# Performance work log

Measured on AMD Instinct MI355X. Metric: run time of the kernel, lower is better.

## Reference

```python
import math
import jax, jax.numpy as jnp
from jax import lax
import numpy as np

B, DIM, H, W = 8, 256, 64, 64
D_STATE, D_CONV, EXPAND = 16, 4, 2
D_INNER = EXPAND * DIM
DT_RANK = math.ceil(DIM / 16)
POS_LEN = 16
EPS = 1e-5
GN_GROUPS = 32


def setup_inputs() -> dict:
    key = jax.random.key(0)
    ks = iter(jax.random.split(key, 24))
    rn = lambda shape, s=0.02: jax.random.normal(next(ks), shape, jnp.float32) * s
    inp = {}
    inp["x"] = jax.random.normal(next(ks), (B, DIM, H, W), jnp.float32)
    inp["pos_emb"] = rn((1, DIM, POS_LEN), 1.0)
    inp["ln_g"] = jnp.ones((DIM,), jnp.float32)
    inp["ln_b"] = jnp.zeros((DIM,), jnp.float32)
    inp["m_in_w"] = rn((2, 2 * D_INNER, DIM))
    inp["m_conv_w"] = rn((2, D_INNER, D_CONV), 0.1)
    inp["m_conv_b"] = jnp.zeros((2, D_INNER), jnp.float32)
    inp["m_xproj_w"] = rn((2, DT_RANK + 2 * D_STATE, D_INNER))
    inp["m_dt_w"] = rn((2, D_INNER, DT_RANK), 0.1)
    inp["m_dt_b"] = rn((2, D_INNER), 0.1)
    inp["m_A_log"] = jnp.tile(jnp.log(jnp.arange(1, D_STATE + 1, dtype=jnp.float32))[None, None, :], (2, D_INNER, 1))
    inp["m_D"] = jnp.ones((2, D_INNER), jnp.float32)
    inp["m_out_w"] = rn((2, DIM, D_INNER))
    inp["proj_w"] = rn((DIM, 2 * DIM))
    inp["proj_b"] = jnp.zeros((DIM,), jnp.float32)
    inp["up_dw_w"] = rn((DIM, 1, 3, 3), 0.1)
    inp["up_bn1_g"] = jnp.ones((DIM,), jnp.float32)
    inp["up_bn1_b"] = jnp.zeros((DIM,), jnp.float32)
    inp["up_pw_w"] = rn((DIM, DIM), 0.05)
    inp["up_bn2_g"] = jnp.ones((DIM,), jnp.float32)
    inp["up_bn2_b"] = jnp.zeros((DIM,), jnp.float32)
    inp["down_pw_w"] = rn((DIM, DIM), 0.05)
    inp["down_bn_g"] = jnp.ones((DIM,), jnp.float32)
    inp["down_bn_b"] = jnp.zeros((DIM,), jnp.float32)
    inp["gn_g"] = jnp.ones((DIM,), jnp.float32)
    inp["gn_b"] = jnp.zeros((DIM,), jnp.float32)
    return inp


def reference(x, pos_emb, ln_g, ln_b, m_in_w, m_conv_w, m_conv_b, m_xproj_w, m_dt_w, m_dt_b,
              m_A_log, m_D, m_out_w, proj_w, proj_b, up_dw_w, up_bn1_g, up_bn1_b, up_pw_w,
              up_bn2_g, up_bn2_b, down_pw_w, down_bn_g, down_bn_b, gn_g, gn_b):
    Bx, C, Hh, Ww = x.shape

    def ln(t):  # LayerNorm over last dim (shared self.norm)
        m = jnp.mean(t, -1, keepdims=True)
        v = jnp.mean((t - m) ** 2, -1, keepdims=True)
        return (t - m) * lax.rsqrt(v + EPS) * ln_g + ln_b

    def bn(t, g, b):  # BatchNorm2d in eval mode with default running stats (mean 0, var 1)
        return t * (g / jnp.sqrt(1.0 + EPS))[None, :, None, None] + b[None, :, None, None]

    def gn(t):  # GroupNorm(32, C), shared params (self.bn)
        Bn, Cn, Hn, Wn = t.shape
        tg = t.reshape(Bn, GN_GROUPS, Cn // GN_GROUPS, Hn, Wn)
        m = jnp.mean(tg, (2, 3, 4), keepdims=True)
        v = jnp.mean((tg - m) ** 2, (2, 3, 4), keepdims=True)
        tg = (tg - m) * lax.rsqrt(v + EPS)
        return tg.reshape(Bn, Cn, Hn, Wn) * gn_g[None, :, None, None] + gn_b[None, :, None, None]

    def interp_pos(N):  # F.interpolate(pos_embed, size=N, mode='linear', align_corners=False)
        coords = jnp.maximum((jnp.arange(N, dtype=jnp.float32) + 0.5) * (POS_LEN / N) - 0.5, 0.0)
        i0 = jnp.floor(coords).astype(jnp.int32)
        i1 = jnp.minimum(i0 + 1, POS_LEN - 1)
        wgt = coords - i0.astype(jnp.float32)
        return pos_emb[:, :, i0] * (1.0 - wgt) + pos_emb[:, :, i1] * wgt  # (1,C,N)

    def pe_branch(vals, idx, N):  # vals (B,C,N); indices interp at same size = identity
        t = vals + interp_pos(N) + idx.astype(jnp.float32)
        return ln(jnp.swapaxes(t, 1, 2))  # (B,N,C)

    def mamba(u, d):  # standard mamba_ssm selective scan; u (B,L,C)
        xz = jnp.einsum('blc,ic->bli', u, m_in_w[d])
        xh, zg = jnp.split(xz, 2, -1)
        xc = lax.conv_general_dilated(jnp.swapaxes(xh, 1, 2), m_conv_w[d][:, None, :], (1,),
                                      [(D_CONV - 1, 0)], feature_group_count=D_INNER,
                                      dimension_numbers=('NCH', 'OIH', 'NCH'))
        xc = jnp.swapaxes(jax.nn.silu(xc + m_conv_b[d][None, :, None]), 1, 2)  # (B,L,di)
        dbl = jnp.einsum('bld,ed->ble', xc, m_xproj_w[d])
        dt = dbl[..., :DT_RANK]
        Bm = dbl[..., DT_RANK:DT_RANK + D_STATE]
        Cm = dbl[..., DT_RANK + D_STATE:]
        dt = jax.nn.softplus(jnp.einsum('blr,dr->bld', dt, m_dt_w[d]) + m_dt_b[d])  # (B,L,di)
        A = -jnp.exp(m_A_log[d])  # (di,ds)
        dA = jnp.exp(dt[..., None] * A)  # (B,L,di,ds)
        dBx = dt[..., None] * Bm[:, :, None, :] * xc[..., None]

        def step(h, inps):
            dA_t, dBx_t, C_t = inps
            h = dA_t * h + dBx_t
            return h, jnp.einsum('bds,bs->bd', h, C_t)

        h0 = jnp.zeros((u.shape[0], D_INNER, D_STATE), u.dtype)
        _, ys = lax.scan(step, h0, (jnp.swapaxes(dA, 0, 1), jnp.swapaxes(dBx, 0, 1), jnp.swapaxes(Cm, 0, 1)))
        y = jnp.swapaxes(ys, 0, 1) + xc * m_D[d]
        y = y * jax.nn.silu(zg)
        return jnp.einsum('bld,od->blo', y, m_out_w[d])

    # z branch: depthwise ConvTranspose2d(k3,s2,p1,op1) + BN + ReLU + pw conv + BN, then ReLU6
    z = lax.conv_general_dilated(x, jnp.flip(up_dw_w, (2, 3)), (1, 1), [(1, 2), (1, 2)],
                                 lhs_dilation=(2, 2), feature_group_count=C,
                                 dimension_numbers=('NCHW', 'OIHW', 'NCHW'))  # (B,C,2H,2W)
    z = jax.nn.relu(bn(z, up_bn1_g, up_bn1_b))
    z = jnp.einsum('bchw,oc->bohw', z, up_pw_w)
    z = jnp.clip(bn(z, up_bn2_g, up_bn2_b), 0.0, 6.0)

    col_max = pe_branch(jnp.max(x, 2), jnp.argmax(x, 2), Ww)
    col_min = pe_branch(jnp.min(x, 2), jnp.argmin(x, 2), Ww)
    row_max = pe_branch(jnp.max(x, 3), jnp.argmax(x, 3), Hh)
    row_min = pe_branch(jnp.min(x, 3), jnp.argmin(x, 3), Hh)
    result_max = jnp.concatenate([col_max, row_max], 1)  # (B, W+H, C)
    result_min = jnp.concatenate([col_min, row_min], 1)

    fm_max = ln(mamba(result_max, 0))
    fm_min = ln(mamba(result_min, 0))
    bm_max = ln(mamba(jnp.flip(result_max, 1), 1))
    bm_min = ln(mamba(jnp.flip(result_min, 1), 1))

    res_max = jnp.concatenate([fm_max, jnp.flip(bm_max, 1)], -1) @ proj_w.T + proj_b
    res_min = jnp.concatenate([fm_min, jnp.flip(bm_min, 1)], -1) @ proj_w.T + proj_b
    res_max = ln(res_max)[:, :, None, :]  # (B,L,1,C)
    res_min = ln(res_min)[:, None, :, :]  # (B,1,L,C)

    res = jnp.transpose(res_max + res_min, (0, 3, 1, 2))  # (B,C,L,L), L=H+W=2H
    res = jnp.clip(res + 3.0, 0.0, 6.0) / 6.0 * z  # h_sigmoid gate
    res = gn(res)
    res = jnp.einsum('bchw,oc->bohw', res[:, :, ::2, ::2], down_pw_w)  # pw conv stride 2
    res = bn(res, down_bn_g, down_bn_b)
    res = gn(res)
    res = res + x
    res = gn(res)
    return res
```

## Files before the change

kernel.cpp:

```cpp
#include <hip/hip_runtime.h>
#include <hip/hip_bf16.h>
#include <math.h>

typedef __hip_bfloat16 bf16;
typedef __attribute__((ext_vector_type(8))) short short8_t;
typedef __attribute__((ext_vector_type(4))) short short4_t;
typedef __attribute__((ext_vector_type(4))) float f32x4_t;

#define EPSV 1e-5f
#define BNSC 0.99999500003749968f

__device__ __forceinline__ float bf2f(bf16 v){ return __bfloat162float(v); }
__device__ __forceinline__ bf16 f2bf(float v){ return __float2bfloat16(v); }

__device__ __forceinline__ float blk_sum(float v, float* sm){
  int tid = threadIdx.x;
  #pragma unroll
  for(int o=32;o>0;o>>=1) v += __shfl_down(v, o, 64);
  if((tid&63)==0) sm[tid>>6] = v;
  __syncthreads();
  float s = 0.f;
  int nw = blockDim.x>>6;
  for(int i=0;i<nw;i++) s += sm[i];
  __syncthreads();
  return s;
}

__device__ __forceinline__ float softplusf(float x){
  return (x > 20.f) ? x : __logf(1.f + __expf(x));
}
__device__ __forceinline__ float siluf(float x){
  return x / (1.f + __expf(-x));
}

__global__ void prep_weights(const float* __restrict__ in_w, const float* __restrict__ out_w,
                             const float* __restrict__ pw_w, const float* __restrict__ dpw_w,
                             const float* __restrict__ proj_w,
                             bf16* __restrict__ Winb, bf16* __restrict__ Woutb,
                             bf16* __restrict__ Wub, bf16* __restrict__ Wdb,
                             float* __restrict__ PT, float* __restrict__ gacc){
  int idx = blockIdx.x*256 + threadIdx.x;
  if(idx < 1536) gacc[idx] = 0.f;
  if(idx < 524288){ Winb[idx] = f2bf(in_w[idx]); return; }
  if(idx < 786432){ int i=idx-524288; Woutb[i] = f2bf(out_w[i]); return; }
  if(idx < 851968){ int i=idx-786432; Wub[i] = f2bf(pw_w[i]); return; }
  if(idx < 917504){ int i=idx-851968; Wdb[i] = f2bf(dpw_w[i]); return; }
  int k = idx - 917504;
  int i = k >> 9, j = k & 511;
  PT[j*256 + i] = proj_w[k];
}

__global__ __launch_bounds__(256)
void r1_reduce_pe(const float* __restrict__ x, const float* __restrict__ pe,
                  float* __restrict__ pmax, float* __restrict__ pmin){
  __shared__ float tile[64*65];
  int bc = blockIdx.x;
  int b = bc >> 8, c = bc & 255;
  const float* xp = x + ((size_t)bc << 12);
  for(int i=threadIdx.x; i<4096; i+=256)
    tile[(i>>6)*65 + (i&63)] = xp[i];
  __syncthreads();
  int wv = threadIdx.x >> 6, t = threadIdx.x & 63;
  if(wv >= 2) return;
  float coords = fmaxf((t + 0.5f)*0.25f - 0.5f, 0.f);
  int i0 = (int)floorf(coords);
  int i1 = min(i0+1, 15);
  float wg = coords - (float)i0;
  float pos = pe[c*16+i0]*(1.f-wg) + pe[c*16+i1]*wg;
  if(wv == 0){
    float cmx=-3.4e38f, cmn=3.4e38f; int cax=0, can=0;
    for(int h=0;h<64;h++){
      float v = tile[h*65 + t];
      if(v > cmx){ cmx=v; cax=h; }
      if(v < cmn){ cmn=v; can=h; }
    }
    size_t base_col = ((size_t)b*128 + t)*256 + c;
    pmax[base_col] = cmx + pos + (float)cax;
    pmin[base_col] = cmn + pos + (float)can;
  } else {
    float rmx=-3.4e38f, rmn=3.4e38f; int rax=0, ran=0;
    for(int w=0;w<64;w++){
      float v = tile[t*65 + w];
      if(v > rmx){ rmx=v; rax=w; }
      if(v < rmn){ rmn=v; ran=w; }
    }
    size_t base_row = ((size_t)b*128 + 64 + t)*256 + c;
    pmax[base_row] = rmx + pos + (float)rax;
    pmin[base_row] = rmn + pos + (float)ran;
  }
}

__global__ void ln_rows2(float* __restrict__ bufA, float* __restrict__ bufB,
                         const float* __restrict__ g, const float* __restrict__ bb,
                         bf16* __restrict__ boutA, bf16* __restrict__ boutB){
  __shared__ float sm[8];
  int row = blockIdx.x, t = threadIdx.x;
  float* buf; bf16* bout;
  if(row < 1024){ buf = bufA; bout = boutA; }
  else { buf = bufB; bout = boutB; row -= 1024; }
  float v = buf[(size_t)row*256 + t];
  float m = blk_sum(v, sm) * (1.f/256.f);
  float dv = v - m;
  float var = blk_sum(dv*dv, sm) * (1.f/256.f);
  float r = dv * rsqrtf(var + EPSV) * g[t] + bb[t];
  buf[(size_t)row*256 + t] = r;
  if(bout) bout[(size_t)row*256 + t] = f2bf(r);
}

__global__ __launch_bounds__(256,2)
void m1_mfma(const bf16* __restrict__ ubmax, const bf16* __restrict__ ubmin,
             const bf16* __restrict__ Win, float* __restrict__ xz){
  __shared__ bf16 att[64*264];
  int bx = blockIdx.x;
  int it = bx & 3, lt = (bx>>2)&1, b = (bx>>3)&7, r = bx>>6;
  int d = r & 1;
  const bf16* u = (r < 2) ? ubmax : ubmin;
  int flip = r & 1;
  int t = threadIdx.x;
  {
    int pr = t>>5, cc = (t&31)*8;
    #pragma unroll
    for(int i=0;i<8;i++){
      int p = pr + i*8;
      int l = lt*64 + p;
      int le = flip ? (127 - l) : l;
      short8_t v = *(const short8_t*)((const short*)u + ((size_t)(b*128 + le))*256 + cc);
      *(short8_t*)&att[p*264 + cc] = v;
    }
  }
  __syncthreads();
  int wv = t>>6, lane = t&63, quad = lane>>4, l16 = lane&15;
  int m0 = wv*64;
  f32x4_t acc[4][4];
  #pragma unroll
  for(int ms=0;ms<4;ms++)
    #pragma unroll
    for(int ns=0;ns<4;ns++) acc[ms][ns] = (f32x4_t){0.f,0.f,0.f,0.f};
  const short* wbase = (const short*)Win + ((size_t)d*1024 + it*256)*256;
  for(int k0=0;k0<256;k0+=32){
    short8_t afr[4], bfr[4];
    #pragma unroll
    for(int ms=0;ms<4;ms++)
      afr[ms] = *(const short8_t*)(wbase + (size_t)(m0 + ms*16 + l16)*256 + k0 + quad*8);
    #pragma unroll
    for(int ns=0;ns<4;ns++)
      bfr[ns] = *(const short8_t*)&att[(ns*16 + l16)*264 + k0 + quad*8];
    #pragma unroll
    for(int ms=0;ms<4;ms++)
      #pragma unroll
      for(int ns=0;ns<4;ns++)
        acc[ms][ns] = __builtin_amdgcn_mfma_f32_16x16x32_bf16(afr[ms], bfr[ns], acc[ms][ns], 0,0,0);
  }
  int rb = r*8 + b;
  #pragma unroll
  for(int ns=0;ns<4;ns++){
    int l = lt*64 + ns*16 + l16;
    float* dst = xz + ((size_t)rb*128 + l)*1024 + it*256;
    #pragma unroll
    for(int ms=0;ms<4;ms++){
      int i = m0 + ms*16 + quad*4;
      *(f32x4_t*)(dst + i) = acc[ms][ns];
    }
  }
}

#define LSEG 8
__global__ __launch_bounds__(256)
void m234(const float* __restrict__ xz, const float* __restrict__ cw,
          const float* __restrict__ cb, const float* __restrict__ xproj,
          const float* __restrict__ dtw, const float* __restrict__ dtbias,
          float* __restrict__ xc, float* __restrict__ dbl, float* __restrict__ dt){
  __shared__ float xzs[(LSEG+3)*512];
  __shared__ float xcs[LSEG*512];
  __shared__ float pbuf[LSEG*96];
  __shared__ float dblrow[LSEG*48];
  int bx = blockIdx.x;
  int rb = bx >> 4, seg = bx & 15;
  int l0 = seg * LSEG;
  int d = (rb >> 3) & 1;
  int t = threadIdx.x;
  #pragma unroll
  for(int j=0; j<(LSEG+3)*512/256; j++){
    int i = t + j*256;
    int r = i >> 9, dd = i & 511;
    int ls = l0 - 3 + r;
    xzs[i] = (ls >= 0) ? xz[((size_t)rb*128 + ls)*1024 + dd] : 0.f;
  }
  __syncthreads();
  #pragma unroll
  for(int j=0; j<(LSEG*512)/256; j++){
    int i = t + j*256;
    int lr = i >> 9, dd = i & 511;
    f32x4_t wv = *(const f32x4_t*)(cw + (size_t)(d*512 + dd)*4);
    float s = cb[d*512 + dd];
    s += xzs[(lr+0)*512 + dd]*wv[0];
    s += xzs[(lr+1)*512 + dd]*wv[1];
    s += xzs[(lr+2)*512 + dd]*wv[2];
    s += xzs[(lr+3)*512 + dd]*wv[3];
    s = siluf(s);
    xcs[i] = s;
    xc[((size_t)(rb*128 + l0 + lr))*512 + dd] = s;
  }
  __syncthreads();
  #pragma unroll
  for(int j=0; j<3; j++){
    int id = t + j*256;
    int row = id / 96;
    int rem = id - row*96;
    int e = rem >> 1, part = rem & 1;
    const float* wp = xproj + ((size_t)(d*48 + e)*512) + part*256;
    const float* xr = xcs + row*512 + part*256;
    float s = 0.f;
    #pragma unroll 4
    for(int k4=0; k4<64; k4++){
      f32x4_t wv = *(const f32x4_t*)(wp + k4*4);
      f32x4_t xv = *(const f32x4_t*)(xr + k4*4);
      s += wv[0]*xv[0] + wv[1]*xv[1] + wv[2]*xv[2] + wv[3]*xv[3];
    }
    pbuf[id] = s;
  }
  __syncthreads();
  for(int i=t; i<LSEG*48; i+=256){
    float s = pbuf[2*i] + pbuf[2*i+1];
    dblrow[i] = s;
    int row = i / 48, e = i - row*48;
    dbl[((size_t)(rb*128 + l0 + row))*48 + e] = s;
  }
  __syncthreads();
  #pragma unroll
  for(int j=0; j<(LSEG*512)/256; j++){
    int i = t + j*256;
    int row = i >> 9, dd = i & 511;
    const float* wp = dtw + (size_t)(d*512 + dd)*16;
    const float* dr = dblrow + row*48;
    float s = dtbias[d*512 + dd];
    #pragma unroll
    for(int r4=0; r4<4; r4++){
      f32x4_t wv = *(const f32x4_t*)(wp + r4*4);
      s += dr[r4*4+0]*wv[0] + dr[r4*4+1]*wv[1] + dr[r4*4+2]*wv[2] + dr[r4*4+3]*wv[3];
    }
    dt[((size_t)(rb*128 + l0 + row))*512 + dd] = softplusf(s);
  }
}

__global__ void m5_passA(const float* __restrict__ dt, const float* __restrict__ xc,
                         const float* __restrict__ dbl, const float* __restrict__ Alog,
                         float* __restrict__ P, float* __restrict__ Hl){
  int bx = blockIdx.x;
  int seg = bx & 7, half = (bx>>3)&1, rb = bx>>4;
  int dd = half*256 + threadIdx.x;
  int d = (rb>>3)&1;
  float A[16], h[16], pr[16];
  #pragma unroll
  for(int s=0;s<16;s++){
    A[s] = -__expf(Alog[(size_t)(d*512 + dd)*16 + s]);
    h[s] = 0.f; pr[s] = 1.f;
  }
  int l0 = seg*16;
  for(int l=l0;l<l0+16;l++){
    size_t row = (size_t)rb*128 + l;
    float dtv = dt[row*512 + dd];
    float xcv = xc[row*512 + dd];
    float bx_ = dtv*xcv;
    const float* dr = dbl + row*48;
    #pragma unroll
    for(int s=0;s<16;s++){
      float dA = __expf(dtv*A[s]);
      pr[s] *= dA;
      h[s] = dA*h[s] + bx_*dr[16+s];
    }
  }
  size_t o = ((size_t)(rb*8 + seg)*512 + dd)*16;
  #pragma unroll
  for(int s=0;s<16;s+=4){
    *(f32x4_t*)(P  + o + s) = (f32x4_t){pr[s],pr[s+1],pr[s+2],pr[s+3]};
    *(f32x4_t*)(Hl + o + s) = (f32x4_t){h[s],h[s+1],h[s+2],h[s+3]};
  }
}

__global__ void m5_passB(const float* __restrict__ dt, const float* __restrict__ xc,
                         const float* __restrict__ dbl, const float* __restrict__ xz,
                         const float* __restrict__ Alog, const float* __restrict__ Dp,
                         const float* __restrict__ P, const float* __restrict__ Hl,
                         bf16* __restrict__ ybb){
  int bx = blockIdx.x;
  int seg = bx & 7, half = (bx>>3)&1, rb = bx>>4;
  int dd = half*256 + threadIdx.x;
  int d = (rb>>3)&1;
  float A[16], h[16];
  #pragma unroll
  for(int s=0;s<16;s++){
    A[s] = -__expf(Alog[(size_t)(d*512 + dd)*16 + s]);
    h[s] = 0.f;
  }
  for(int j=0;j<seg;j++){
    size_t o = ((size_t)(rb*8 + j)*512 + dd)*16;
    #pragma unroll
    for(int s=0;s<16;s+=4){
      f32x4_t pv = *(const f32x4_t*)(P + o + s);
      f32x4_t hv = *(const f32x4_t*)(Hl + o + s);
      h[s]   = pv[0]*h[s]   + hv[0];
      h[s+1] = pv[1]*h[s+1] + hv[1];
      h[s+2] = pv[2]*h[s+2] + hv[2];
      h[s+3] = pv[3]*h[s+3] + hv[3];
    }
  }
  float Dv = Dp[d*512 + dd];
  int l0 = seg*16;
  for(int l=l0;l<l0+16;l++){
    size_t row = (size_t)rb*128 + l;
    float dtv = dt[row*512 + dd];
    float xcv = xc[row*512 + dd];
    float zgv = xz[row*1024 + 512 + dd];
    const float* dr = dbl + row*48;
    float bx_ = dtv*xcv;
    float y = 0.f;
    #pragma unroll
    for(int s=0;s<16;s++){
      h[s] = __expf(dtv*A[s])*h[s] + bx_*dr[16+s];
      y += h[s]*dr[32+s];
    }
    ybb[row*512 + dd] = f2bf((y + xcv*Dv) * siluf(zgv));
  }
}

__global__ __launch_bounds__(256,2)
void m6_mfma(const bf16* __restrict__ ybb, const bf16* __restrict__ Wout,
             const float* __restrict__ lng, const float* __restrict__ lnb,
             float* __restrict__ mo){
  __shared__ char smem[64*264*4];
  bf16* ybt = (bf16*)smem;
  float* fbuf = (float*)smem;
  int bx = blockIdx.x;
  int lt = bx & 1, b = (bx>>1)&7, r = bx>>4;
  int d = r & 1, rb = r*8 + b;
  size_t rowbase = (size_t)rb*128 + lt*64;
  int t = threadIdx.x;
  for(int i=t;i<4096;i+=256){
    int row = i>>6, c8 = (i&63)*8;
    short8_t v = *(const short8_t*)((const short*)ybb + (rowbase + row)*512 + c8);
    *(short8_t*)&ybt[row*520 + c8] = v;
  }
  __syncthreads();
  int wv = t>>6, lane = t&63, quad = lane>>4, l16 = lane&15;
  int m0 = wv*64;
  f32x4_t acc[4][4];
  #pragma unroll
  for(int ms=0;ms<4;ms++)
    #pragma unroll
    for(int ns=0;ns<4;ns++) acc[ms][ns] = (f32x4_t){0.f,0.f,0.f,0.f};
  const short* wbase = (const short*)Wout + (size_t)d*256*512;
  for(int k0=0;k0<512;k0+=32){
    short8_t afr[4], bfr[4];
    #pragma unroll
    for(int ms=0;ms<4;ms++)
      afr[ms] = *(const short8_t*)(wbase + (size_t)(m0 + ms*16 + l16)*512 + k0 + quad*8);
    #pragma unroll
    for(int ns=0;ns<4;ns++)
      bfr[ns] = *(const short8_t*)&ybt[(ns*16 + l16)*520 + k0 + quad*8];
    #pragma unroll
    for(int ms=0;ms<4;ms++)
      #pragma unroll
      for(int ns=0;ns<4;ns++)
        acc[ms][ns] = __builtin_amdgcn_mfma_f32_16x16x32_bf16(afr[ms], bfr[ns], acc[ms][ns], 0,0,0);
  }
  __syncthreads();
  #pragma unroll
  for(int ns=0;ns<4;ns++){
    int row = ns*16 + l16;
    #pragma unroll
    for(int ms=0;ms<4;ms++){
      int o = m0 + ms*16 + quad*4;
      *(f32x4_t*)(fbuf + row*264 + o) = acc[ms][ns];
    }
  }
  __syncthreads();
  {
    int row = t >> 2, part = t & 3;
    const float* fr = fbuf + row*264;
    float s = 0.f;
    #pragma unroll 8
    for(int j=0;j<64;j++){
      int col = part*64 + ((j + part*16) & 63);
      s += fr[col];
    }
    s += __shfl_xor(s, 1, 64);
    s += __shfl_xor(s, 2, 64);
    float m = s * (1.f/256.f);
    float q = 0.f;
    #pragma unroll 8
    for(int j=0;j<64;j++){
      int col = part*64 + ((j + part*16) & 63);
      float dv = fr[col] - m;
      q += dv*dv;
    }
    q += __shfl_xor(q, 1, 64);
    q += __shfl_xor(q, 2, 64);
    float rs = rsqrtf(q*(1.f/256.f) + EPSV);
    float* dst = mo + (rowbase + row)*256;
    for(int j=0;j<64;j++){
      int col = part*64 + j;
      dst[col] = (fr[col] - m)*rs*lng[col] + lnb[col];
    }
  }
}

__global__ void m7_proj(const float* __restrict__ mo, const float* __restrict__ PT,
                        const float* __restrict__ pb, const float* __restrict__ lng,
                        const float* __restrict__ lnb, float* __restrict__ resm,
                        float* __restrict__ resn){
  __shared__ float ct[16*512];
  __shared__ float fbuf[16*264];
  int bx = blockIdx.x;
  int tt = bx >> 6, rem = bx & 63, b = rem >> 3, lt = rem & 7;
  int fr_ = tt*2, br = tt*2 + 1;
  for(int i=threadIdx.x;i<16*512;i+=256){
    int lr = i >> 9, k = i & 511;
    int l = lt*16 + lr;
    ct[i] = (k < 256)
      ? mo[(((size_t)(fr_*8+b)*128) + l)*256 + k]
      : mo[(((size_t)(br*8+b)*128) + (127-l))*256 + (k-256)];
  }
  __syncthreads();
  float acc[16];
  #pragma unroll
  for(int q=0;q<16;q++) acc[q] = 0.f;
  int t = threadIdx.x;
  for(int k=0;k<512;k++){
    float pv = PT[(size_t)k*256 + t];
    #pragma unroll
    for(int q=0;q<16;q++) acc[q] += pv * ct[(q<<9) + k];
  }
  float bias = pb[t];
  #pragma unroll
  for(int q=0;q<16;q++) fbuf[q*264 + t] = acc[q] + bias;
  __syncthreads();
  float* dstbuf = tt ? resn : resm;
  if(t < 64){
    int row = t >> 2, part = t & 3;
    const float* fr = fbuf + row*264;
    float s = 0.f;
    for(int j=0;j<64;j++){
      int col = part*64 + ((j + part*16) & 63);
      s += fr[col];
    }
    s += __shfl_xor(s, 1, 64);
    s += __shfl_xor(s, 2, 64);
    float m = s * (1.f/256.f);
    float q = 0.f;
    for(int j=0;j<64;j++){
      int col = part*64 + ((j + part*16) & 63);
      float dv = fr[col] - m;
      q += dv*dv;
    }
    q += __shfl_xor(q, 1, 64);
    q += __shfl_xor(q, 2, 64);
    float rs = rsqrtf(q*(1.f/256.f) + EPSV);
    float* dst = dstbuf + ((size_t)b*128 + lt*16 + row)*256;
    for(int j=0;j<64;j++){
      int col = part*64 + j;
      dst[col] = (fr[col] - m)*rs*lng[col] + lnb[col];
    }
  }
}

__global__ __launch_bounds__(256)
void k1_deconv_T(const float* __restrict__ x, const float* __restrict__ wdw,
                 const float* __restrict__ g1, const float* __restrict__ b1,
                 bf16* __restrict__ zT){
  __shared__ float in[2*64*33];
  __shared__ bf16 ot[64*80];
  int bx = blockIdx.x;
  int cb = bx & 3, half = (bx>>2)&1, h = (bx>>3)&127, b = bx>>10;
  int c0 = cb*64, w0 = half*64, iw0 = w0>>1;
  int h_odd = h & 1;
  int ihA = h_odd ? (h-1)>>1 : h>>1;
  int ihB = (h+1)>>1;
  bool hasB = h_odd && (ihB < 64);
  for(int i = threadIdx.x; i < 4224; i += 256){
    int row = i / 2112;
    int rem = i - row*2112;
    int c = rem / 33;
    int iw = rem - c*33;
    int ihl = row ? ihB : ihA;
    bool valid = (iw0 + iw < 64) && (row == 0 || hasB);
    in[i] = valid ? x[(((size_t)b*256 + c0 + c)<<12) + (ihl<<6) + iw0 + iw] : 0.f;
  }
  __syncthreads();
  int c = threadIdx.x & 63, g = threadIdx.x >> 6;
  const float* wp = wdw + (c0+c)*9;
  int khA3 = h_odd ? 6 : 3;
  float wA0 = wp[khA3], wA1 = wp[khA3+1], wA2 = wp[khA3+2];
  float wB0 = wp[0],    wB1 = wp[1],      wB2 = wp[2];
  float scale = g1[c0+c]*BNSC, bias = b1[c0+c];
  const float* inA = in + c*33;
  const float* inB = in + 2112 + c*33;
  #pragma unroll
  for(int i=0;i<16;i++){
    int wi = g*16 + i;
    float s;
    if(!(i&1)){
      int iw = wi>>1;
      s = inA[iw]*wA1 + inB[iw]*wB1;
    } else {
      int iwa = (wi-1)>>1, iwb = (wi+1)>>1;
      s = inA[iwa]*wA2 + inA[iwb]*wA0 + inB[iwa]*wB2 + inB[iwb]*wB0;
    }
    ot[wi*80 + c] = f2bf(fmaxf(s*scale + bias, 0.f));
  }
  __syncthreads();
  int rr = threadIdx.x >> 3;
  int co = (threadIdx.x & 7) * 8;
  size_t obase = (((size_t)b*16384) + (size_t)h*128 + w0)*256 + c0;
  #pragma unroll
  for(int pass=0; pass<2; pass++){
    int wi = rr + pass*32;
    short8_t v = *(const short8_t*)&ot[wi*80 + co];
    *(short8_t*)((short*)zT + obase + (size_t)wi*256 + co) = v;
  }
}

__global__ __launch_bounds__(256,2)
void k2_mfma(const bf16* __restrict__ zT, const bf16* __restrict__ Wub,
             const float* __restrict__ g2, const float* __restrict__ b2,
             const float* __restrict__ resm, const float* __restrict__ resn,
             bf16* __restrict__ resS, float* __restrict__ gsum1, float* __restrict__ gssq1){
  __shared__ bf16 zt[128*264];
  __shared__ float rm_s[256];
  __shared__ float gn_s[32], gn_q[32];
  int b = blockIdx.y;
  int p0 = blockIdx.x*128;
  int h = p0 >> 7;
  int t = threadIdx.x;
  if(t < 32){ gn_s[t] = 0.f; gn_q[t] = 0.f; }
  if(t >= 64 && t < 128){
    int tt = t - 64;
    *(f32x4_t*)&rm_s[tt*4] = *(const f32x4_t*)(resm + ((size_t)b*128 + h)*256 + tt*4);
  }
  {
    const short* src = (const short*)zT + (((size_t)b*16384 + p0)*256);
    int pr = t>>5;
    int cc = (t&31)*8;
    #pragma unroll
    for(int i=0;i<16;i++){
      int p = pr + i*8;
      short8_t v = *(const short8_t*)(src + (size_t)p*256 + cc);
      *(short8_t*)&zt[p*264 + cc] = v;
    }
  }
  __syncthreads();
  int wv = t>>6, lane = t&63, quad = lane>>4, l16 = lane&15;
  int m0 = wv*64;
  f32x4_t acc[4][8];
  #pragma unroll
  for(int ms=0;ms<4;ms++)
    #pragma unroll
    for(int ns=0;ns<8;ns++) acc[ms][ns] = (f32x4_t){0.f,0.f,0.f,0.f};
  const short* wp = (const short*)Wub + (size_t)(m0 + l16)*256 + quad*8;
  short8_t afr[4];
  #pragma unroll
  for(int ms=0;ms<4;ms++) afr[ms] = *(const short8_t*)(wp + (size_t)ms*16*256);
  for(int k0=0;k0<256;k0+=32){
    short8_t anext[4];
    if(k0 + 32 < 256){
      #pragma unroll
      for(int ms=0;ms<4;ms++)
        anext[ms] = *(const short8_t*)(wp + (size_t)ms*16*256 + k0 + 32);
    }
    short8_t bfr[8];
    #pragma unroll
    for(int ns=0;ns<8;ns++)
      bfr[ns] = *(const short8_t*)&zt[(ns*16 + l16)*264 + k0 + quad*8];
    #pragma unroll
    for(int ms=0;ms<4;ms++)
      #pragma unroll
      for(int ns=0;ns<8;ns++)
        acc[ms][ns] = __builtin_amdgcn_mfma_f32_16x16x32_bf16(afr[ms], bfr[ns], acc[ms][ns], 0,0,0);
    #pragma unroll
    for(int ms=0;ms<4;ms++) afr[ms] = anext[ms];
  }
  __syncthreads();
  bool h_even = ((h & 1) == 0);
  float sg[4], qg[4];
  #pragma unroll
  for(int ms=0;ms<4;ms++){ sg[ms]=0.f; qg[ms]=0.f; }
  #pragma unroll
  for(int ns=0;ns<8;ns++){
    int pl = ns*16 + l16;
    const float* rn = resn + ((size_t)b*128 + pl)*256;
    bool store = h_even && ((pl & 1) == 0);
    #pragma unroll
    for(int ms=0;ms<4;ms++){
      int o = m0 + ms*16 + quad*4;
      f32x4_t a = acc[ms][ns];
      f32x4_t gv = *(const f32x4_t*)(g2+o);
      f32x4_t bv = *(const f32x4_t*)(b2+o);
      f32x4_t rmv = *(const f32x4_t*)&rm_s[o];
      f32x4_t rnv = *(const f32x4_t*)(rn+o);
      alignas(8) bf16 ov[4];
      #pragma unroll
      for(int r=0;r<4;r++){
        float zv = a[r]*(gv[r]*BNSC) + bv[r];
        zv = fminf(fmaxf(zv, 0.f), 6.f);
        float gate = fminf(fmaxf(rmv[r]+rnv[r]+3.f, 0.f), 6.f)*(1.f/6.f);
        float vo = zv*gate;
        ov[r] = f2bf(vo);
        sg[ms] += vo;
        qg[ms] += vo*vo;
      }
      if(store) *(short4_t*)&zt[pl*264 + o] = *(const short4_t*)ov;
    }
  }
  #pragma unroll
  for(int ms=0;ms<4;ms++){
    float S = sg[ms], Q = qg[ms];
    S += __shfl_xor(S, 1, 64);  Q += __shfl_xor(Q, 1, 64);
    S += __shfl_xor(S, 2, 64);  Q += __shfl_xor(Q, 2, 64);
    S += __shfl_xor(S, 4, 64);  Q += __shfl_xor(Q, 4, 64);
    S += __shfl_xor(S, 8, 64);  Q += __shfl_xor(Q, 8, 64);
    if(l16 == 0){
      int o = m0 + ms*16 + quad*4;
      atomicAdd(&gn_s[o>>3], S);
      atomicAdd(&gn_q[o>>3], Q);
    }
  }
  __syncthreads();
  if(t < 32){
    atomicAdd(&gsum1[b*32 + t], gn_s[t]);
    atomicAdd(&gssq1[b*32 + t], gn_q[t]);
  }
  if(h_even){
    short* dst = (short*)resS + ((size_t)b*4096 + (h>>1)*64)*256;
    #pragma unroll
    for(int it=0; it<8; it++){
      int slot = t + it*256;
      int row = slot >> 5;
      int co = (slot & 31)*8;
      short8_t v = *(const short8_t*)&zt[(row*2)*264 + co];
      *(short8_t*)(dst + (size_t)row*256 + co) = v;
    }
  }
}

__global__ __launch_bounds__(256,2)
void k4_mfma(const bf16* __restrict__ resS, const bf16* __restrict__ Wdb,
             const float* __restrict__ gsum1, const float* __restrict__ gssq1,
             const float* __restrict__ gng, const float* __restrict__ gnb,
             const float* __restrict__ dbg, const float* __restrict__ dbb,
             float* __restrict__ t1, float* __restrict__ gsum2, float* __restrict__ gssq2){
  __shared__ bf16 at[128*264];
  __shared__ float sc[256], sb[256];
  __shared__ float stm[32], str[32];
  int b = blockIdx.y;
  int q0 = blockIdx.x*128;
  int t = threadIdx.x;
  if(t < 32){
    float m = gsum1[b*32+t] * (1.f/131072.f);
    float var = gssq1[b*32+t] * (1.f/131072.f) - m*m;
    stm[t] = m;
    str[t] = rsqrtf(var + EPSV);
  }
  __syncthreads();
  {
    int cch = t, g = cch>>3;
    float m = stm[g], rs = str[g];
    float s = rs*gng[cch];
    sc[cch] = s; sb[cch] = gnb[cch] - m*s;
  }
  __syncthreads();
  {
    int pr = t>>5;
    int cc = (t&31)*8;
    const short* src = (const short*)resS + ((size_t)b*4096 + q0)*256;
    #pragma unroll
    for(int i=0;i<16;i++){
      int q = pr + i*8;
      short8_t v = *(const short8_t*)(src + (size_t)q*256 + cc);
      const bf16* vv = (const bf16*)&v;
      alignas(16) bf16 ov[8];
      #pragma unroll
      for(int j=0;j<8;j++) ov[j] = f2bf(bf2f(vv[j])*sc[cc+j] + sb[cc+j]);
      *(short8_t*)&at[q*264 + cc] = *(const short8_t*)ov;
    }
  }
  __syncthreads();
  int wv = t>>6, lane = t&63, quad = lane>>4, l16 = lane&15;
  int n0 = wv*64;
  f32x4_t acc[8][4];
  #pragma unroll
  for(int ms=0;ms<8;ms++)
    #pragma unroll
    for(int ns=0;ns<4;ns++) acc[ms][ns] = (f32x4_t){0.f,0.f,0.f,0.f};
  const short* wp = (const short*)Wdb + (size_t)(n0 + l16)*256 + quad*8;
  short8_t bfr[4];
  #pragma unroll
  for(int ns=0;ns<4;ns++) bfr[ns] = *(const short8_t*)(wp + (size_t)ns*16*256);
  for(int k0=0;k0<256;k0+=32){
    short8_t bnext[4];
    if(k0 + 32 < 256){
      #pragma unroll
      for(int ns=0;ns<4;ns++)
        bnext[ns] = *(const short8_t*)(wp + (size_t)ns*16*256 + k0 + 32);
    }
    short8_t afr[8];
    #pragma unroll
    for(int ms=0;ms<8;ms++)
      afr[ms] = *(const short8_t*)&at[(ms*16 + l16)*264 + k0 + quad*8];
    #pragma unroll
    for(int ms=0;ms<8;ms++)
      #pragma unroll
      for(int ns=0;ns<4;ns++)
        acc[ms][ns] = __builtin_amdgcn_mfma_f32_16x16x32_bf16(afr[ms], bfr[ns], acc[ms][ns], 0,0,0);
    #pragma unroll
    for(int ns=0;ns<4;ns++) bfr[ns] = bnext[ns];
  }
  #pragma unroll
  for(int ns=0;ns<4;ns++){
    int o = n0 + ns*16 + l16;
    float s2 = dbg[o]*BNSC, bb2 = dbb[o];
    float* dst = t1 + (((size_t)b*256 + o) << 12);
    float s_=0.f, q_=0.f;
    #pragma unroll
    for(int ms=0;ms<8;ms++){
      int ps = q0 + ms*16 + quad*4;
      f32x4_t a = acc[ms][ns];
      f32x4_t ov;
      #pragma unroll
      for(int r=0;r<4;r++){
        ov[r] = a[r]*s2 + bb2;
        s_ += ov[r];
        q_ += ov[r]*ov[r];
      }
      *(f32x4_t*)(dst + ps) = ov;
    }
    #pragma unroll
    for(int msk=1; msk<=4; msk<<=1){
      s_ += __shfl_xor(s_, msk, 64);
      q_ += __shfl_xor(q_, msk, 64);
    }
    s_ += __shfl_xor(s_, 16, 64);
    q_ += __shfl_xor(q_, 16, 64);
    s_ += __shfl_xor(s_, 32, 64);
    q_ += __shfl_xor(q_, 32, 64);
    if(((l16 & 7) == 0) && (quad == 0)){
      atomicAdd(&gsum2[b*32 + (o>>3)], s_);
      atomicAdd(&gssq2[b*32 + (o>>3)], q_);
    }
  }
}

__global__ void k6_gn_add(float* __restrict__ t1, const float* __restrict__ x,
                          const float* __restrict__ gsum2, const float* __restrict__ gssq2,
                          const float* __restrict__ gng, const float* __restrict__ gnb,
                          float* __restrict__ gsum3, float* __restrict__ gssq3){
  __shared__ float sm[8];
  int i4 = blockIdx.x*256 + threadIdx.x;
  int idx = i4 << 2;
  int c = (idx >> 12) & 255, b = idx >> 20, g = c >> 3;
  float m2 = gsum2[b*32+g] * (1.f/32768.f);
  float var = gssq2[b*32+g] * (1.f/32768.f) - m2*m2;
  float rs = rsqrtf(var + EPSV);
  float scl = rs*gng[c], off = gnb[c] - m2*scl;
  f32x4_t tv = *(const f32x4_t*)(t1 + idx);
  f32x4_t xv = *(const f32x4_t*)(x + idx);
  f32x4_t ov;
  float S = 0.f, Q = 0.f;
  #pragma unroll
  for(int r=0;r<4;r++){
    float v = tv[r]*scl + off + xv[r];
    ov[r] = v;
    S += v; Q += v*v;
  }
  *(f32x4_t*)(t1 + idx) = ov;
  S = blk_sum(S, sm);
  Q = blk_sum(Q, sm);
  if(threadIdx.x == 0){
    atomicAdd(&gsum3[b*32 + g], S);
    atomicAdd(&gssq3[b*32 + g], Q);
  }
}

__global__ void k8_gn_out(const float* __restrict__ t1, const float* __restrict__ gsum3,
                          const float* __restrict__ gssq3, const float* __restrict__ gng,
                          const float* __restrict__ gnb, float* __restrict__ out){
  int i4 = blockIdx.x*256 + threadIdx.x;
  int idx = i4 << 2;
  int c = (idx >> 12) & 255, b = idx >> 20, g = c >> 3;
  float m = gsum3[b*32+g] * (1.f/32768.f);
  float var = gssq3[b*32+g] * (1.f/32768.f) - m*m;
  float rs = rsqrtf(var + EPSV);
  float scl = rs*gng[c], off = gnb[c] - m*scl;
  f32x4_t tv = *(const f32x4_t*)(t1 + idx);
  f32x4_t ov;
  #pragma unroll
  for(int r=0;r<4;r++) ov[r] = tv[r]*scl + off;
  *(f32x4_t*)(out + idx) = ov;
}

extern "C" void kernel_launch(void* const* d_in, const int* in_sizes, int n_in,
                              void* d_out, int out_size, void* d_ws, size_t ws_size,
                              hipStream_t stream){
  const float* x      = (const float*)d_in[0];
  const float* pos    = (const float*)d_in[1];
  const float* ln_g   = (const float*)d_in[2];
  const float* ln_b   = (const float*)d_in[3];
  const float* in_w   = (const float*)d_in[4];
  const float* conv_w = (const float*)d_in[5];
  const float* conv_b = (const float*)d_in[6];
  const float* xproj  = (const float*)d_in[7];
  const float* dt_w   = (const float*)d_in[8];
  const float* dt_b   = (const float*)d_in[9];
  const float* A_log  = (const float*)d_in[10];
  const float* Dp     = (const float*)d_in[11];
  const float* out_w  = (const float*)d_in[12];
  const float* proj_w = (const float*)d_in[13];
  const float* proj_b = (const float*)d_in[14];
  const float* dw_w   = (const float*)d_in[15];
  const float* bn1g   = (const float*)d_in[16];
  const float* bn1b   = (const float*)d_in[17];
  const float* pw_w   = (const float*)d_in[18];
  const float* bn2g   = (const float*)d_in[19];
  const float* bn2b   = (const float*)d_in[20];
  const float* dpw_w  = (const float*)d_in[21];
  const float* dbng   = (const float*)d_in[22];
  const float* dbnb   = (const float*)d_in[23];
  const float* gng    = (const float*)d_in[24];
  const float* gnb    = (const float*)d_in[25];
  float* out = (float*)d_out;

  float* ws = (float*)d_ws;
  bf16*  resS = (bf16*)ws;
  bf16*  zT   = (bf16*)(ws + 16777216);
  float* scanP = ws + 16777216;
  float* scanH = ws + 16777216 + 2097152;
  float* zone = ws + 33554432;
  float* xz   = zone;
  float* xc   = xz  + 4194304;
  float* dbl  = xc  + 2097152;
  float* dtb  = dbl + 196608;
  bf16*  ybb  = (bf16*)(dtb + 2097152);
  float* t1   = zone;
  float* mo   = zone + 9633792;
  float* resm = mo   + 1048576;
  float* resn = resm + 262144;
  float* pmax = resn + 262144;
  float* pmin = pmax + 262144;
  float* PT   = pmin + 262144;
  bf16*  ubmax= (bf16*)(PT + 131072);
  bf16*  ubmin= (bf16*)(PT + 131072 + 131072);
  bf16*  Winb = (bf16*)(PT + 131072 + 262144);
  bf16*  Woutb= (bf16*)(PT + 131072 + 524288);
  bf16*  Wub  = (bf16*)(PT + 131072 + 655360);
  bf16*  Wdb  = (bf16*)(PT + 131072 + 688128);
  float* gacc = PT + 131072 + 720896;
  float* gsum1 = gacc,        *gssq1 = gacc + 256;
  float* gsum2 = gacc + 512,  *gssq2 = gacc + 768;
  float* gsum3 = gacc + 1024, *gssq3 = gacc + 1280;

  prep_weights<<<4096,256,0,stream>>>(in_w, out_w, pw_w, dpw_w, proj_w,
                                      Winb, Woutb, Wub, Wdb, PT, gacc);

  r1_reduce_pe<<<2048,256,0,stream>>>(x, pos, pmax, pmin);
  ln_rows2<<<2048,256,0,stream>>>(pmax, pmin, ln_g, ln_b, ubmax, ubmin);

  m1_mfma<<<256,256,0,stream>>>(ubmax, ubmin, Winb, xz);
  m234<<<512,256,0,stream>>>(xz, conv_w, conv_b, xproj, dt_w, dt_b, xc, dbl, dtb);
  m5_passA<<<512,256,0,stream>>>(dtb, xc, dbl, A_log, scanP, scanH);
  m5_passB<<<512,256,0,stream>>>(dtb, xc, dbl, xz, A_log, Dp, scanP, scanH, ybb);
  m6_mfma<<<64,256,0,stream>>>(ybb, Woutb, ln_g, ln_b, mo);
  m7_proj<<<128,256,0,stream>>>(mo, PT, proj_b, ln_g, ln_b, resm, resn);

  k1_deconv_T<<<8192,256,0,stream>>>(x, dw_w, bn1g, bn1b, zT);
  k2_mfma<<<dim3(128,8),256,0,stream>>>(zT, Wub, bn2g, bn2b, resm, resn, resS,
                                        gsum1, gssq1);

  k4_mfma<<<dim3(32,8),256,0,stream>>>(resS, Wdb, gsum1, gssq1,
                                       gng, gnb, dbng, dbnb, t1, gsum2, gssq2);

  k6_gn_add<<<8192,256,0,stream>>>(t1, x, gsum2, gssq2, gng, gnb, gsum3, gssq3);
  k8_gn_out<<<8192,256,0,stream>>>(t1, gsum3, gssq3, gng, gnb, out);
}
```

Baseline: 502.4 us.

## Derive final GroupNorm stats algebraically and split conv/xproj kernel into finer segments

The separate residual-add plus GroupNorm pass (k6) is removed. Per-channel sums of x are computed in the first reduction kernel, and per-channel sums, squares and cross products with x are gathered in k4. A small compose kernel then derives the second and third GroupNorm statistics in closed form, so the final kernel writes out = A*t1 + B*x + C in one pass. Separately, m234 now uses 4-row segments with 1024 blocks and reads the conv taps straight from global memory, and xproj uses 4 partial sums per row instead of 2. The algebraic variance form may lose some precision, and there are more atomics per channel.

```diff
diff --git a/kernel.cpp b/kernel.cpp
--- a/kernel.cpp
+++ b/kernel.cpp
@@ -40,7 +40,7 @@
                              bf16* __restrict__ Wub, bf16* __restrict__ Wdb,
                              float* __restrict__ PT, float* __restrict__ gacc){
   int idx = blockIdx.x*256 + threadIdx.x;
-  if(idx < 1536) gacc[idx] = 0.f;
+  if(idx < 6656) gacc[idx] = 0.f;
   if(idx < 524288){ Winb[idx] = f2bf(in_w[idx]); return; }
   if(idx < 786432){ int i=idx-524288; Woutb[i] = f2bf(out_w[i]); return; }
   if(idx < 851968){ int i=idx-786432; Wub[i] = f2bf(pw_w[i]); return; }
@@ -52,15 +52,28 @@
 
 __global__ __launch_bounds__(256)
 void r1_reduce_pe(const float* __restrict__ x, const float* __restrict__ pe,
-                  float* __restrict__ pmax, float* __restrict__ pmin){
+                  float* __restrict__ pmax, float* __restrict__ pmin,
+                  float* __restrict__ xs, float* __restrict__ xq){
   __shared__ float tile[64*65];
+  __shared__ float rs_[4], rq_[4];
   int bc = blockIdx.x;
   int b = bc >> 8, c = bc & 255;
   const float* xp = x + ((size_t)bc << 12);
-  for(int i=threadIdx.x; i<4096; i+=256)
-    tile[(i>>6)*65 + (i&63)] = xp[i];
-  __syncthreads();
+  float s = 0.f, q = 0.f;
+  for(int i=threadIdx.x; i<4096; i+=256){
+    float v = xp[i];
+    tile[(i>>6)*65 + (i&63)] = v;
+    s += v; q += v*v;
+  }
+  #pragma unroll
+  for(int o=32;o>0;o>>=1){ s += __shfl_down(s, o, 64); q += __shfl_down(q, o, 64); }
   int wv = threadIdx.x >> 6, t = threadIdx.x & 63;
+  if(t == 0){ rs_[wv] = s; rq_[wv] = q; }
+  __syncthreads();
+  if(threadIdx.x == 0){
+    xs[bc] = rs_[0]+rs_[1]+rs_[2]+rs_[3];
+    xq[bc] = rq_[0]+rq_[1]+rq_[2]+rq_[3];
+  }
   if(wv >= 2) return;
   float coords = fmaxf((t + 0.5f)*0.25f - 0.5f, 0.f);
   int i0 = (int)floorf(coords);
@@ -164,55 +177,49 @@
   }
 }
 
-#define LSEG 8
+#define LSEG4 4
 __global__ __launch_bounds__(256)
 void m234(const float* __restrict__ xz, const float* __restrict__ cw,
           const float* __restrict__ cb, const float* __restrict__ xproj,
           const float* __restrict__ dtw, const float* __restrict__ dtbias,
           float* __restrict__ xc, float* __restrict__ dbl, float* __restrict__ dt){
-  __shared__ float xzs[(LSEG+3)*512];
-  __shared__ float xcs[LSEG*512];
-  __shared__ float pbuf[LSEG*96];
-  __shared__ float dblrow[LSEG*48];
+  __shared__ float xcs[LSEG4*512];
+  __shared__ float pbuf[LSEG4*48*4];
+  __shared__ float dblrow[LSEG4*48];
   int bx = blockIdx.x;
-  int rb = bx >> 4, seg = bx & 15;
-  int l0 = seg * LSEG;
+  int rb = bx >> 5, seg = bx & 31;
+  int l0 = seg * LSEG4;
   int d = (rb >> 3) & 1;
   int t = threadIdx.x;
   #pragma unroll
-  for(int j=0; j<(LSEG+3)*512/256; j++){
-    int i = t + j*256;
-    int r = i >> 9, dd = i & 511;
-    int ls = l0 - 3 + r;
-    xzs[i] = (ls >= 0) ? xz[((size_t)rb*128 + ls)*1024 + dd] : 0.f;
-  }
-  __syncthreads();
-  #pragma unroll
-  for(int j=0; j<(LSEG*512)/256; j++){
+  for(int j=0; j<(LSEG4*512)/256; j++){
     int i = t + j*256;
     int lr = i >> 9, dd = i & 511;
+    int gl = l0 + lr;
+    const float* src = xz + ((size_t)rb*128 + gl)*1024 + dd;
     f32x4_t wv = *(const f32x4_t*)(cw + (size_t)(d*512 + dd)*4);
     float s = cb[d*512 + dd];
-    s += xzs[(lr+0)*512 + dd]*wv[0];
-    s += xzs[(lr+1)*512 + dd]*wv[1];
-    s += xzs[(lr+2)*512 + dd]*wv[2];
-    s += xzs[(lr+3)*512 + dd]*wv[3];
+    float v0 = (gl >= 3) ? src[-3*1024] : 0.f;
+    float v1 = (gl >= 2) ? src[-2*1024] : 0.f;
+    float v2 = (gl >= 1) ? src[-1*1024] : 0.f;
+    float v3 = src[0];
+    s += v0*wv[0] + v1*wv[1] + v2*wv[2] + v3*wv[3];
     s = siluf(s);
     xcs[i] = s;
-    xc[((size_t)(rb*128 + l0 + lr))*512 + dd] = s;
+    xc[((size_t)(rb*128 + gl))*512 + dd] = s;
   }
   __syncthreads();
   #pragma unroll
   for(int j=0; j<3; j++){
     int id = t + j*256;
-    int row = id / 96;
-    int rem = id - row*96;
-    int e = rem >> 1, part = rem & 1;
-    const float* wp = xproj + ((size_t)(d*48 + e)*512) + part*256;
-    const float* xr = xcs + row*512 + part*256;
+    int row = id / 192;
+    int rem = id - row*192;
+    int e = rem >> 2, part = rem & 3;
+    const float* wp = xproj + ((size_t)(d*48 + e)*512) + part*128;
+    const float* xr = xcs + row*512 + part*128;
     float s = 0.f;
     #pragma unroll 4
-    for(int k4=0; k4<64; k4++){
+    for(int k4=0; k4<32; k4++){
       f32x4_t wv = *(const f32x4_t*)(wp + k4*4);
       f32x4_t xv = *(const f32x4_t*)(xr + k4*4);
       s += wv[0]*xv[0] + wv[1]*xv[1] + wv[2]*xv[2] + wv[3]*xv[3];
@@ -220,15 +227,16 @@
     pbuf[id] = s;
   }
   __syncthreads();
-  for(int i=t; i<LSEG*48; i+=256){
-    float s = pbuf[2*i] + pbuf[2*i+1];
+  for(int i=t; i<LSEG4*48; i+=256){
+    int row = i / 48, e = i - row*48;
+    int base = row*192 + e*4;
+    float s = pbuf[base] + pbuf[base+1] + pbuf[base+2] + pbuf[base+3];
     dblrow[i] = s;
-    int row = i / 48, e = i - row*48;
     dbl[((size_t)(rb*128 + l0 + row))*48 + e] = s;
   }
   __syncthreads();
   #pragma unroll
-  for(int j=0; j<(LSEG*512)/256; j++){
+  for(int j=0; j<(LSEG4*512)/256; j++){
     int i = t + j*256;
     int row = i >> 9, dd = i & 511;
     const float* wp = dtw + (size_t)(d*512 + dd)*16;
@@ -647,7 +655,8 @@
              const float* __restrict__ gsum1, const float* __restrict__ gssq1,
              const float* __restrict__ gng, const float* __restrict__ gnb,
              const float* __restrict__ dbg, const float* __restrict__ dbb,
-             float* __restrict__ t1, float* __restrict__ gsum2, float* __restrict__ gssq2){
+             const float* __restrict__ x, float* __restrict__ t1,
+             float* __restrict__ t1s, float* __restrict__ t1q, float* __restrict__ t1x){
   __shared__ bf16 at[128*264];
   __shared__ float sc[256], sb[256];
   __shared__ float stm[32], str[32];
@@ -719,81 +728,83 @@
     int o = n0 + ns*16 + l16;
     float s2 = dbg[o]*BNSC, bb2 = dbb[o];
     float* dst = t1 + (((size_t)b*256 + o) << 12);
-    float s_=0.f, q_=0.f;
+    const float* xsrc = x + (((size_t)b*256 + o) << 12);
+    float s_=0.f, q_=0.f, c_=0.f;
     #pragma unroll
     for(int ms=0;ms<8;ms++){
       int ps = q0 + ms*16 + quad*4;
       f32x4_t a = acc[ms][ns];
+      f32x4_t xv = *(const f32x4_t*)(xsrc + ps);
       f32x4_t ov;
       #pragma unroll
       for(int r=0;r<4;r++){
         ov[r] = a[r]*s2 + bb2;
         s_ += ov[r];
         q_ += ov[r]*ov[r];
+        c_ += ov[r]*xv[r];
       }
       *(f32x4_t*)(dst + ps) = ov;
     }
-    #pragma unroll
-    for(int msk=1; msk<=4; msk<<=1){
-      s_ += __shfl_xor(s_, msk, 64);
-      q_ += __shfl_xor(q_, msk, 64);
-    }
     s_ += __shfl_xor(s_, 16, 64);
     q_ += __shfl_xor(q_, 16, 64);
+    c_ += __shfl_xor(c_, 16, 64);
     s_ += __shfl_xor(s_, 32, 64);
     q_ += __shfl_xor(q_, 32, 64);
-    if(((l16 & 7) == 0) && (quad == 0)){
-      atomicAdd(&gsum2[b*32 + (o>>3)], s_);
-      atomicAdd(&gssq2[b*32 + (o>>3)], q_);
-    }
-  }
-}
-
-__global__ void k6_gn_add(float* __restrict__ t1, const float* __restrict__ x,
-                          const float* __restrict__ gsum2, const float* __restrict__ gssq2,
-                          const float* __restrict__ gng, const float* __restrict__ gnb,
-                          float* __restrict__ gsum3, float* __restrict__ gssq3){
-  __shared__ float sm[8];
+    c_ += __shfl_xor(c_, 32, 64);
+    if(quad == 0){
+      atomicAdd(&t1s[b*256 + o], s_);
+      atomicAdd(&t1q[b*256 + o], q_);
+      atomicAdd(&t1x[b*256 + o], c_);
+    }
+  }
+}
+
+__global__ void compose_gn(const float* __restrict__ t1s, const float* __restrict__ t1q,
+                           const float* __restrict__ t1x, const float* __restrict__ xs,
+                           const float* __restrict__ xq, const float* __restrict__ gng,
+                           const float* __restrict__ gnb,
+                           float* __restrict__ cA, float* __restrict__ cB, float* __restrict__ cC){
+  int b = blockIdx.x, c = threadIdx.x;
+  int i = b*256 + c;
+  float ts = t1s[i], tq = t1q[i], tx = t1x[i];
+  float sx = xs[i], qx = xq[i];
+  float gs = ts, gq = tq;
+  gs += __shfl_xor(gs,1,64); gq += __shfl_xor(gq,1,64);
+  gs += __shfl_xor(gs,2,64); gq += __shfl_xor(gq,2,64);
+  gs += __shfl_xor(gs,4,64); gq += __shfl_xor(gq,4,64);
+  float m2 = gs*(1.f/32768.f);
+  float v2 = gq*(1.f/32768.f) - m2*m2;
+  float rs2 = rsqrtf(v2 + EPSV);
+  float a  = rs2*gng[c];
+  float bb = gnb[c] - m2*a;
+  float Su = a*ts + 4096.f*bb + sx;
+  float Qu = a*a*tq + 4096.f*bb*bb + qx + 2.f*a*bb*ts + 2.f*a*tx + 2.f*bb*sx;
+  float gSu = Su, gQu = Qu;
+  gSu += __shfl_xor(gSu,1,64); gQu += __shfl_xor(gQu,1,64);
+  gSu += __shfl_xor(gSu,2,64); gQu += __shfl_xor(gQu,2,64);
+  gSu += __shfl_xor(gSu,4,64); gQu += __shfl_xor(gQu,4,64);
+  float m3 = gSu*(1.f/32768.f);
+  float v3 = gQu*(1.f/32768.f) - m3*m3;
+  float rs3 = rsqrtf(v3 + EPSV);
+  float s3 = rs3*gng[c];
+  cA[i] = a*s3;
+  cB[i] = s3;
+  cC[i] = (bb - m3)*s3 + gnb[c];
+}
+
+__global__ void k8_gn_out(const float* __restrict__ t1, const float* __restrict__ x,
+                          const float* __restrict__ cA, const float* __restrict__ cB,
+                          const float* __restrict__ cC, float* __restrict__ out){
   int i4 = blockIdx.x*256 + threadIdx.x;
   int idx = i4 << 2;
-  int c = (idx >> 12) & 255, b = idx >> 20, g = c >> 3;
-  float m2 = gsum2[b*32+g] * (1.f/32768.f);
-  float var = gssq2[b*32+g] * (1.f/32768.f) - m2*m2;
-  float rs = rsqrtf(var + EPSV);
-  float scl = rs*gng[c], off = gnb[c] - m2*scl;
+  int c = (idx >> 12) & 255, b = idx >> 20;
+  int i = b*256 + c;
+  float A = cA[i], Bv = cB[i], C = cC[i];
   f32x4_t tv = *(const f32x4_t*)(t1 + idx);
   f32x4_t xv = *(const f32x4_t*)(x + idx);
   f32x4_t ov;
-  float S = 0.f, Q = 0.f;
-  #pragma unroll
-  for(int r=0;r<4;r++){
-    float v = tv[r]*scl + off + xv[r];
-    ov[r] = v;
-    S += v; Q += v*v;
-  }
-  *(f32x4_t*)(t1 + idx) = ov;
-  S = blk_sum(S, sm);
-  Q = blk_sum(Q, sm);
-  if(threadIdx.x == 0){
-    atomicAdd(&gsum3[b*32 + g], S);
-    atomicAdd(&gssq3[b*32 + g], Q);
-  }
-}
-
-__global__ void k8_gn_out(const float* __restrict__ t1, const float* __restrict__ gsum3,
-                          const float* __restrict__ gssq3, const float* __restrict__ gng,
-                          const float* __restrict__ gnb, float* __restrict__ out){
-  int i4 = blockIdx.x*256 + threadIdx.x;
-  int idx = i4 << 2;
-  int c = (idx >> 12) & 255, b = idx >> 20, g = c >> 3;
-  float m = gsum3[b*32+g] * (1.f/32768.f);
-  float var = gssq3[b*32+g] * (1.f/32768.f) - m*m;
-  float rs = rsqrtf(var + EPSV);
-  float scl = rs*gng[c], off = gnb[c] - m*scl;
-  f32x4_t tv = *(const f32x4_t*)(t1 + idx);
-  f32x4_t ov;
-  #pragma unroll
-  for(int r=0;r<4;r++) ov[r] = tv[r]*scl + off;
+  #pragma unroll
+  for(int r=0;r<4;r++) ov[r] = A*tv[r] + Bv*xv[r] + C;
   *(f32x4_t*)(out + idx) = ov;
 }
 
@@ -854,17 +865,23 @@
   bf16*  Wdb  = (bf16*)(PT + 131072 + 688128);
   float* gacc = PT + 131072 + 720896;
   float* gsum1 = gacc,        *gssq1 = gacc + 256;
-  float* gsum2 = gacc + 512,  *gssq2 = gacc + 768;
-  float* gsum3 = gacc + 1024, *gssq3 = gacc + 1280;
+  float* t1s = gacc + 512;
+  float* t1q = gacc + 2560;
+  float* t1x = gacc + 4608;
+  float* xs  = gacc + 6656;
+  float* xq  = gacc + 8704;
+  float* cA  = gacc + 10752;
+  float* cB  = gacc + 12800;
+  float* cC  = gacc + 14848;
 
   prep_weights<<<4096,256,0,stream>>>(in_w, out_w, pw_w, dpw_w, proj_w,
                                       Winb, Woutb, Wub, Wdb, PT, gacc);
 
-  r1_reduce_pe<<<2048,256,0,stream>>>(x, pos, pmax, pmin);
+  r1_reduce_pe<<<2048,256,0,stream>>>(x, pos, pmax, pmin, xs, xq);
   ln_rows2<<<2048,256,0,stream>>>(pmax, pmin, ln_g, ln_b, ubmax, ubmin);
 
   m1_mfma<<<256,256,0,stream>>>(ubmax, ubmin, Winb, xz);
-  m234<<<512,256,0,stream>>>(xz, conv_w, conv_b, xproj, dt_w, dt_b, xc, dbl, dtb);
+  m234<<<1024,256,0,stream>>>(xz, conv_w, conv_b, xproj, dt_w, dt_b, xc, dbl, dtb);
   m5_passA<<<512,256,0,stream>>>(dtb, xc, dbl, A_log, scanP, scanH);
   m5_passB<<<512,256,0,stream>>>(dtb, xc, dbl, xz, A_log, Dp, scanP, scanH, ybb);
   m6_mfma<<<64,256,0,stream>>>(ybb, Woutb, ln_g, ln_b, mo);
@@ -875,8 +892,8 @@
                                         gsum1, gssq1);
 
   k4_mfma<<<dim3(32,8),256,0,stream>>>(resS, Wdb, gsum1, gssq1,
-                                       gng, gnb, dbng, dbnb, t1, gsum2, gssq2);
-
-  k6_gn_add<<<8192,256,0,stream>>>(t1, x, gsum2, gssq2, gng, gnb, gsum3, gssq3);
-  k8_gn_out<<<8192,256,0,stream>>>(t1, gsum3, gssq3, gng, gnb, out);
-}
+                                       gng, gnb, dbng, dbnb, x, t1, t1s, t1q, t1x);
+
+  compose_gn<<<8,256,0,stream>>>(t1s, t1q, t1x, xs, xq, gng, gnb, cA, cB, cC);
+  k8_gn_out<<<8192,256,0,stream>>>(t1, x, cA, cB, cC, out);
+}
```

After: 485.1 us. -3.4%, faster.
